# Kernel optimization log

Hardware: AMD Instinct MI355X
Metric: run time of the kernel (lower is better)

The kernel has to match this reference:

```python
import jax, jax.numpy as jnp
import numpy as np

D_MODEL = 1024
NUM_HEADS = 16
HEAD_DIM = D_MODEL // NUM_HEADS
B, S = 4, 2048


def _xavier(key, shape, gain=0.1):
    fan_in, fan_out = shape[1], shape[0]
    a = gain * np.sqrt(6.0 / (fan_in + fan_out))
    return jax.random.uniform(key, shape, jnp.float32, -a, a)


def setup_inputs() -> dict:
    key = jax.random.key(0)
    ks = jax.random.split(key, 11)
    inp = {
        "q": jax.random.normal(ks[0], (B, S, D_MODEL), jnp.float32),
        "k": jax.random.normal(ks[1], (B, S, D_MODEL), jnp.float32),
        "v": jax.random.normal(ks[2], (B, S, D_MODEL), jnp.float32),
        # nn.Linear weights are [out, in]; y = x @ W.T + b
        "Wq": _xavier(ks[3], (D_MODEL, D_MODEL)),
        "bq": jnp.zeros((D_MODEL,), jnp.float32),
        "Wk": _xavier(ks[4], (D_MODEL, D_MODEL)),
        "bk": jnp.zeros((D_MODEL,), jnp.float32),
        "Wv": _xavier(ks[5], (D_MODEL, D_MODEL)),
        "bv": jnp.zeros((D_MODEL,), jnp.float32),
        "Wo": _xavier(ks[6], (D_MODEL, D_MODEL)),
        "bo": jnp.zeros((D_MODEL,), jnp.float32),
    }
    return inp


def reference(q, k, v, Wq, bq, Wk, bk, Wv, bv, Wo, bo):
    b = q.shape[0]
    qh = (q @ Wq.T + bq).reshape(b, -1, NUM_HEADS, HEAD_DIM).transpose(0, 2, 1, 3)
    kh = (k @ Wk.T + bk).reshape(b, -1, NUM_HEADS, HEAD_DIM).transpose(0, 2, 1, 3)
    vh = (v @ Wv.T + bv).reshape(b, -1, NUM_HEADS, HEAD_DIM).transpose(0, 2, 1, 3)
    # NOTE: original (buggy) module scales by sqrt(d_model), not sqrt(head_dim)
    scale = 1.0 / jnp.sqrt(jnp.float32(D_MODEL))
    scores = jnp.einsum('bhqd,bhkd->bhqk', qh, kh) * scale  # [B,H,S,S]
    attn = jax.nn.softmax(scores, axis=-1)
    out = jnp.einsum('bhqk,bhkd->bhqd', attn, vh)
    out = out.transpose(0, 2, 1, 3).reshape(b, -1, D_MODEL)
    return out @ Wo.T + bo
```

## Files before the change

kernel.cpp:

```cpp
#include <hip/hip_runtime.h>

typedef unsigned short u16;
typedef short bf16x8 __attribute__((ext_vector_type(8)));
typedef float f32x4 __attribute__((ext_vector_type(4)));
typedef u16 u16x8 __attribute__((ext_vector_type(8)));

__device__ __forceinline__ u16 f2bf(float f) {
  unsigned u = __float_as_uint(f);
  u = u + 0x7fffu + ((u >> 16) & 1u);
  return (u16)(u >> 16);
}

__device__ __forceinline__ float fexp2(float x) {
#if __has_builtin(__builtin_amdgcn_exp2f)
  return __builtin_amdgcn_exp2f(x);
#else
  return exp2f(x);
#endif
}

#define GLD16(ldsp, gp)                                                         \
  __builtin_amdgcn_global_load_lds(                                             \
      (__attribute__((address_space(1))) void*)(void*)(gp),                     \
      (__attribute__((address_space(3))) void*)(ldsp), 16, 0, 0)

#define CVTPK(dst, lo, hi)                                                      \
  asm("v_cvt_pk_bf16_f32 %0, %1, %2" : "=v"(dst) : "v"(lo), "v"(hi))
#define PACK8(dst, a0, a1, a2, a3, a4, a5, a6, a7)                              \
  do {                                                                          \
    union { unsigned u_[4]; bf16x8 v_; } c_;                                    \
    CVTPK(c_.u_[0], a0, a1); CVTPK(c_.u_[1], a2, a3);                           \
    CVTPK(c_.u_[2], a4, a5); CVTPK(c_.u_[3], a6, a7);                           \
    dst = c_.v_;                                                                \
  } while (0)

__global__ __launch_bounds__(256) void pack_w4(const float* __restrict__ w0,
                                               const float* __restrict__ w1,
                                               const float* __restrict__ w2,
                                               const float* __restrict__ w3,
                                               u16* __restrict__ out) {
  int i = blockIdx.x * 256 + threadIdx.x;
  int which = i >> 17;
  const float* src = which == 0 ? w0 : which == 1 ? w1 : which == 2 ? w2 : w3;
  int j = i & 131071;
  const float4* p = (const float4*)src + (size_t)j * 2;
  float4 a = p[0], b = p[1];
  u16x8 r;
  r[0] = f2bf(a.x); r[1] = f2bf(a.y); r[2] = f2bf(a.z); r[3] = f2bf(a.w);
  r[4] = f2bf(b.x); r[5] = f2bf(b.y); r[6] = f2bf(b.z); r[7] = f2bf(b.w);
  *(u16x8*)(out + (size_t)i * 8) = r;
}

__global__ __launch_bounds__(256, 2)
void gemm_qkv(const float* __restrict__ qi, const float* __restrict__ ki,
              const float* __restrict__ vi, const u16* __restrict__ wbf,
              const float* __restrict__ bq, const float* __restrict__ bk,
              const float* __restrict__ bv, u16* __restrict__ qo,
              u16* __restrict__ ko, u16* __restrict__ vo) {
  constexpr int K = 1024;
  __shared__ __align__(16) u16 As[128 * 64];
  __shared__ __align__(16) u16 Bs[128 * 64];
  const int z = blockIdx.z;
  const float* Af = z == 0 ? qi : z == 1 ? ki : vi;
  const u16* Bw = wbf + ((size_t)z << 20);
  const float* bias = z == 0 ? bq : z == 1 ? bk : bv;

  const int t = threadIdx.x;
  const int w = t >> 6, l = t & 63;
  const int lr = l & 15, lg = l >> 4;
  const int flat = blockIdx.x | (blockIdx.y << 3);
  const int swz = ((flat & 7) << 6) | (flat >> 3);
  const int row0 = (swz >> 3) * 128, col0 = (swz & 7) * 128;
  const int wm = (w >> 1) * 64, wn = (w & 1) * 64;

  f32x4 acc[4][4] = {};

  const int ar = t >> 3;
  const int xw = ((t & 7) ^ (ar & 7)) * 16;
  const float* gA = Af + (size_t)(row0 + ar) * K + (t & 7) * 8;
  const u16* gB = Bw + (size_t)(col0 + ar) * K + (((t & 7) ^ (ar & 7)) * 8);
  u16* lB = &Bs[w * 512];

  float4 a0[4], a1[4];
#pragma unroll
  for (int j = 0; j < 4; ++j) {
    const float* p = gA + (size_t)j * 32 * K;
    a0[j] = *(const float4*)p;
    a1[j] = *(const float4*)(p + 4);
  }

  for (int kt = 0; kt < 16; ++kt) {
#pragma unroll
    for (int j = 0; j < 4; ++j) {
      bf16x8 c;
      PACK8(c, a0[j].x, a0[j].y, a0[j].z, a0[j].w, a1[j].x, a1[j].y, a1[j].z, a1[j].w);
      *(bf16x8*)((char*)As + (ar + j * 32) * 128 + xw) = c;
    }
#pragma unroll
    for (int j = 0; j < 4; ++j)
      GLD16(lB + j * 2048, gB + (size_t)j * 32 * K + kt * 64);
    if (kt < 15) {
#pragma unroll
      for (int j = 0; j < 4; ++j) {
        const float* p = gA + (size_t)j * 32 * K + (kt + 1) * 64;
        a0[j] = *(const float4*)p;
        a1[j] = *(const float4*)(p + 4);
      }
    }
    __syncthreads();
#pragma unroll
    for (int kh2 = 0; kh2 < 2; ++kh2) {
      bf16x8 aF[4], bF[4];
      const int bc = (kh2 * 64 + lg * 16) ^ ((lr & 7) * 16);
#pragma unroll
      for (int mi = 0; mi < 4; ++mi)
        aF[mi] = *(const bf16x8*)((const char*)As + (wm + mi * 16 + lr) * 128 + bc);
#pragma unroll
      for (int ni = 0; ni < 4; ++ni)
        bF[ni] = *(const bf16x8*)((const char*)Bs + (wn + ni * 16 + lr) * 128 + bc);
#pragma unroll
      for (int mi = 0; mi < 4; ++mi)
#pragma unroll
        for (int ni = 0; ni < 4; ++ni)
          acc[mi][ni] = __builtin_amdgcn_mfma_f32_16x16x32_bf16(aF[mi], bF[ni],
                                                                acc[mi][ni], 0, 0, 0);
    }
    __syncthreads();
  }

#pragma unroll
  for (int mi = 0; mi < 4; ++mi) {
#pragma unroll
    for (int ni = 0; ni < 4; ++ni) {
      const int n = col0 + wn + ni * 16 + lr;
      const float bvv = bias[n];
#pragma unroll
      for (int r = 0; r < 4; ++r) {
        const int m = row0 + wm + mi * 16 + lg * 4 + r;
        const float vv = acc[mi][ni][r] + bvv;
        const int bI = m >> 11, s = m & 2047, h = n >> 6, d = n & 63;
        if (z == 0) {
          qo[((size_t)((bI << 4) + h) * 2048 + s) * 64 + d] = f2bf(vv * 0.045084223f);
        } else if (z == 1) {
          ko[((size_t)((bI << 4) + h) * 2048 + s) * 64 + d] = f2bf(vv);
        } else {
          int bh = (bI << 4) + h, tile = s >> 6, kp = s & 63;
          int kM = kp >> 5, k5 = kp & 31;
          int kpp = kM * 32 + ((k5 >> 2) & 3) * 8 + (k5 >> 4) * 4 + (k5 & 3);
          int chunk = (kpp >> 3) ^ (d & 7);
          vo[((size_t)bh << 17) + tile * 4096 + d * 64 + chunk * 8 + (kpp & 7)] = f2bf(vv);
        }
      }
    }
  }
}

__global__ __launch_bounds__(256, 2)
void gemm_out(const u16* __restrict__ A, const u16* __restrict__ B,
              const float* __restrict__ bias, float* __restrict__ outp) {
  constexpr int K = 1024;
  __shared__ __align__(16) u16 As[128 * 64];
  __shared__ __align__(16) u16 Bs[128 * 64];
  const int t = threadIdx.x;
  const int w = t >> 6;
  const int l = t & 63;
  const int lr = l & 15, lg = l >> 4;
  const int flat = blockIdx.x | (blockIdx.y << 3);
  const int swz = ((flat & 7) << 6) | (flat >> 3);
  const int row0 = (swz >> 3) * 128, col0 = (swz & 7) * 128;
  const int wm = (w >> 1) * 64, wn = (w & 1) * 64;

  f32x4 acc[4][4] = {};

  const int srow = t >> 3;
  const int scol = ((t & 7) ^ (srow & 7)) * 8;
  const u16* gA = A + (size_t)(row0 + srow) * K + scol;
  const u16* gB = B + (size_t)(col0 + srow) * K + scol;
  u16* lA = &As[w * 512];
  u16* lB = &Bs[w * 512];

  for (int k0 = 0; k0 < K; k0 += 64) {
#pragma unroll
    for (int j = 0; j < 4; ++j) {
      GLD16(lA + j * 2048, gA + (size_t)j * 32 * K + k0);
      GLD16(lB + j * 2048, gB + (size_t)j * 32 * K + k0);
    }
    __syncthreads();
#pragma unroll
    for (int kh2 = 0; kh2 < 2; ++kh2) {
      bf16x8 aF[4], bF[4];
      const int bc = (kh2 * 64 + lg * 16) ^ ((lr & 7) * 16);
#pragma unroll
      for (int mi = 0; mi < 4; ++mi)
        aF[mi] = *(const bf16x8*)((const char*)As + (wm + mi * 16 + lr) * 128 + bc);
#pragma unroll
      for (int ni = 0; ni < 4; ++ni)
        bF[ni] = *(const bf16x8*)((const char*)Bs + (wn + ni * 16 + lr) * 128 + bc);
#pragma unroll
      for (int mi = 0; mi < 4; ++mi)
#pragma unroll
        for (int ni = 0; ni < 4; ++ni)
          acc[mi][ni] = __builtin_amdgcn_mfma_f32_16x16x32_bf16(aF[mi], bF[ni],
                                                                acc[mi][ni], 0, 0, 0);
    }
    __syncthreads();
  }

#pragma unroll
  for (int mi = 0; mi < 4; ++mi)
#pragma unroll
    for (int ni = 0; ni < 4; ++ni) {
      const int n = col0 + wn + ni * 16 + lr;
      const float bv = bias[n];
#pragma unroll
      for (int r = 0; r < 4; ++r) {
        const int m = row0 + wm + mi * 16 + lg * 4 + r;
        outp[(size_t)m * 1024 + n] = acc[mi][ni][r] + bv;
      }
    }
}

__global__ __launch_bounds__(256, 3)
void attn_fwd(const u16* __restrict__ qh, const u16* __restrict__ kh,
              const u16* __restrict__ vp, u16* __restrict__ aout) {
  __shared__ __align__(16) u16 Ks[2][4096];
  __shared__ __align__(16) u16 Vl[2][4096];
  const int t = threadIdx.x;
  const int w = t >> 6, l = t & 63;
  const int lr = l & 15, lg = l >> 4;
  const int flat = blockIdx.x | (blockIdx.y << 4);
  const int swz = ((flat & 7) << 7) | (flat >> 3);
  const int qb = swz & 15, bh = swz >> 4;
  const int q0 = qb * 128 + w * 32;

  bf16x8 qf[2][2];
#pragma unroll
  for (int qi = 0; qi < 2; ++qi) {
    const u16* qp = qh + ((size_t)bh * 2048 + q0 + qi * 16 + lr) * 64 + lg * 8;
    qf[qi][0] = *(const bf16x8*)qp;
    qf[qi][1] = *(const bf16x8*)(qp + 32);
  }

  f32x4 o0[4] = {}, o1[4] = {};
  f32x4 sm0 = {}, sm1 = {};
  const bf16x8 ones = {16256, 16256, 16256, 16256, 16256, 16256, 16256, 16256};

  const int krow = t >> 3, kseg = t & 7;
  const u16* gK = kh + ((size_t)bh * 2048 + krow) * 64 + ((kseg ^ (krow & 7)) * 8);
  const u16* gV = vp + ((size_t)bh << 17) + t * 8;

  const int xo0 = (lg * 16) ^ ((lr & 7) * 16);
  const int xo1 = xo0 ^ 64;

  {
    u16* kd = &Ks[0][0] + w * 512;
    u16* vd = &Vl[0][0] + w * 512;
    GLD16(kd, gK); GLD16(kd + 2048, gK + 2048);
    GLD16(vd, gV); GLD16(vd + 2048, gV + 2048);
    gK += 4096; gV += 4096;
  }
  __syncthreads();

  for (int tix = 0; tix < 32; ++tix) {
    const int cur = tix & 1;
    if (tix < 31) {
      u16* kd = &Ks[cur ^ 1][0] + w * 512;
      u16* vd = &Vl[cur ^ 1][0] + w * 512;
      GLD16(kd, gK); GLD16(kd + 2048, gK + 2048);
      GLD16(vd, gV); GLD16(vd + 2048, gV + 2048);
      gK += 4096; gV += 4096;
    }
    const char* kb = (const char*)&Ks[cur][0];
    f32x4 s0[4], s1[4];
    __builtin_amdgcn_s_setprio(1);
#pragma unroll
    for (int cq = 0; cq < 4; ++cq) {
      const char* rowp = kb + (cq * 16 + lr) * 128;
      bf16x8 kf0 = *(const bf16x8*)(rowp + xo0);
      bf16x8 kf1 = *(const bf16x8*)(rowp + xo1);
      f32x4 a = {}, b2 = {};
      a  = __builtin_amdgcn_mfma_f32_16x16x32_bf16(kf0, qf[0][0], a, 0, 0, 0);
      a  = __builtin_amdgcn_mfma_f32_16x16x32_bf16(kf1, qf[0][1], a, 0, 0, 0);
      b2 = __builtin_amdgcn_mfma_f32_16x16x32_bf16(kf0, qf[1][0], b2, 0, 0, 0);
      b2 = __builtin_amdgcn_mfma_f32_16x16x32_bf16(kf1, qf[1][1], b2, 0, 0, 0);
      s0[cq] = a; s1[cq] = b2;
    }
    __builtin_amdgcn_s_setprio(0);
    float p0[16], p1[16];
#pragma unroll
    for (int cq = 0; cq < 4; ++cq)
#pragma unroll
      for (int r = 0; r < 4; ++r) {
        p0[cq * 4 + r] = fexp2(s0[cq][r]);
        p1[cq * 4 + r] = fexp2(s1[cq][r]);
      }
    bf16x8 pA0, pA1, pB0, pB1;
    PACK8(pA0, p0[0], p0[1], p0[2], p0[3], p0[4], p0[5], p0[6], p0[7]);
    PACK8(pA1, p0[8], p0[9], p0[10], p0[11], p0[12], p0[13], p0[14], p0[15]);
    PACK8(pB0, p1[0], p1[1], p1[2], p1[3], p1[4], p1[5], p1[6], p1[7]);
    PACK8(pB1, p1[8], p1[9], p1[10], p1[11], p1[12], p1[13], p1[14], p1[15]);
    __builtin_amdgcn_s_setprio(1);
    sm0 = __builtin_amdgcn_mfma_f32_16x16x32_bf16(pA0, ones, sm0, 0, 0, 0);
    sm0 = __builtin_amdgcn_mfma_f32_16x16x32_bf16(pA1, ones, sm0, 0, 0, 0);
    sm1 = __builtin_amdgcn_mfma_f32_16x16x32_bf16(pB0, ones, sm1, 0, 0, 0);
    sm1 = __builtin_amdgcn_mfma_f32_16x16x32_bf16(pB1, ones, sm1, 0, 0, 0);
    const char* vbb = (const char*)&Vl[cur][0];
#pragma unroll
    for (int dc = 0; dc < 4; ++dc) {
      const char* rp = vbb + (dc * 16 + lr) * 128;
      bf16x8 vA = *(const bf16x8*)(rp + xo0);
      bf16x8 vB = *(const bf16x8*)(rp + xo1);
      o0[dc] = __builtin_amdgcn_mfma_f32_16x16x32_bf16(pA0, vA, o0[dc], 0, 0, 0);
      o0[dc] = __builtin_amdgcn_mfma_f32_16x16x32_bf16(pA1, vB, o0[dc], 0, 0, 0);
      o1[dc] = __builtin_amdgcn_mfma_f32_16x16x32_bf16(pB0, vA, o1[dc], 0, 0, 0);
      o1[dc] = __builtin_amdgcn_mfma_f32_16x16x32_bf16(pB1, vB, o1[dc], 0, 0, 0);
    }
    __builtin_amdgcn_s_setprio(0);
    __syncthreads();
  }

  const int b = bh >> 4, h = bh & 15;
#pragma unroll
  for (int r = 0; r < 4; ++r) {
    const float dA = 1.f / sm0[r];
    const float dB = 1.f / sm1[r];
    const size_t rowA = (size_t)b * 2048 + q0 + lg * 4 + r;
#pragma unroll
    for (int dc = 0; dc < 4; ++dc) {
      aout[rowA * 1024 + h * 64 + dc * 16 + lr] = f2bf(o0[dc][r] * dA);
      aout[(rowA + 16) * 1024 + h * 64 + dc * 16 + lr] = f2bf(o1[dc][r] * dB);
    }
  }
}

extern "C" void kernel_launch(void* const* d_in, const int* in_sizes, int n_in,
                              void* d_out, int out_size, void* d_ws, size_t ws_size,
                              hipStream_t stream) {
  const float* q  = (const float*)d_in[0];
  const float* k  = (const float*)d_in[1];
  const float* v  = (const float*)d_in[2];
  const float* Wq = (const float*)d_in[3];
  const float* bq = (const float*)d_in[4];
  const float* Wk = (const float*)d_in[5];
  const float* bk = (const float*)d_in[6];
  const float* Wv = (const float*)d_in[7];
  const float* bv = (const float*)d_in[8];
  const float* Wo = (const float*)d_in[9];
  const float* bo = (const float*)d_in[10];

  char* ws = (char*)d_ws;
  u16* wbf  = (u16*)(ws);
  u16* aout = (u16*)(ws + (8ull << 20));
  u16* qhB  = (u16*)(ws + (24ull << 20));
  u16* khB  = (u16*)(ws + (40ull << 20));
  u16* vtB  = (u16*)(ws + (56ull << 20));

  pack_w4<<<2048, 256, 0, stream>>>(Wq, Wk, Wv, Wo, wbf);
  gemm_qkv<<<dim3(8, 64, 3), 256, 0, stream>>>(q, k, v, wbf, bq, bk, bv,
                                               qhB, khB, vtB);
  attn_fwd<<<dim3(16, 64), 256, 0, stream>>>(qhB, khB, vtB, aout);
  gemm_out<<<dim3(8, 64), 256, 0, stream>>>(aout, wbf + (3u << 20), bo,
                                            (float*)d_out);

  (void)in_sizes; (void)n_in; (void)out_size; (void)ws_size;
}
```

Before: 172.1 us.

## Pre-convert activations to bf16 and run QKV projections as separate GEMMs

Replaces the fused QKV GEMM, which loaded fp32 activations through registers and packed them to bf16 in-kernel, with a standalone fp32-to-bf16 pack kernel followed by a templated bf16 GEMM per projection. The new GEMM loads both operands directly into LDS with global_load_lds. The intent is a simpler, more latency-tolerant inner loop. The cost is extra global traffic (writing and rereading bf16 activations), six launches instead of one, and the loss of the single 3-way grid, since the three projections now run serially through one shared buffer.

```diff
diff --git a/kernel.cpp b/kernel.cpp
--- a/kernel.cpp
+++ b/kernel.cpp
@@ -33,6 +33,18 @@
     CVTPK(c_.u_[2], a4, a5); CVTPK(c_.u_[3], a6, a7);                           \
     dst = c_.v_;                                                                \
   } while (0)
+
+__global__ __launch_bounds__(256) void pack_bf16(const float* __restrict__ in,
+                                                 u16* __restrict__ out, int n8) {
+  int i = blockIdx.x * blockDim.x + threadIdx.x;
+  if (i >= n8) return;
+  const float4* p = (const float4*)in + (size_t)i * 2;
+  float4 a = p[0], b = p[1];
+  u16x8 r;
+  r[0] = f2bf(a.x); r[1] = f2bf(a.y); r[2] = f2bf(a.z); r[3] = f2bf(a.w);
+  r[4] = f2bf(b.x); r[5] = f2bf(b.y); r[6] = f2bf(b.z); r[7] = f2bf(b.w);
+  *(u16x8*)(out + (size_t)i * 8) = r;
+}
 
 __global__ __launch_bounds__(256) void pack_w4(const float* __restrict__ w0,
                                                const float* __restrict__ w1,
@@ -51,22 +63,17 @@
   *(u16x8*)(out + (size_t)i * 8) = r;
 }
 
+template <int EPI>
 __global__ __launch_bounds__(256, 2)
-void gemm_qkv(const float* __restrict__ qi, const float* __restrict__ ki,
-              const float* __restrict__ vi, const u16* __restrict__ wbf,
-              const float* __restrict__ bq, const float* __restrict__ bk,
-              const float* __restrict__ bv, u16* __restrict__ qo,
-              u16* __restrict__ ko, u16* __restrict__ vo) {
+void gemm_bt(const u16* __restrict__ A, const u16* __restrict__ B,
+             const float* __restrict__ bias, u16* __restrict__ outp,
+             float qscale) {
   constexpr int K = 1024;
   __shared__ __align__(16) u16 As[128 * 64];
   __shared__ __align__(16) u16 Bs[128 * 64];
-  const int z = blockIdx.z;
-  const float* Af = z == 0 ? qi : z == 1 ? ki : vi;
-  const u16* Bw = wbf + ((size_t)z << 20);
-  const float* bias = z == 0 ? bq : z == 1 ? bk : bv;
-
   const int t = threadIdx.x;
-  const int w = t >> 6, l = t & 63;
+  const int w = t >> 6;
+  const int l = t & 63;
   const int lr = l & 15, lg = l >> 4;
   const int flat = blockIdx.x | (blockIdx.y << 3);
   const int swz = ((flat & 7) << 6) | (flat >> 3);
@@ -75,37 +82,18 @@
 
   f32x4 acc[4][4] = {};
 
-  const int ar = t >> 3;
-  const int xw = ((t & 7) ^ (ar & 7)) * 16;
-  const float* gA = Af + (size_t)(row0 + ar) * K + (t & 7) * 8;
-  const u16* gB = Bw + (size_t)(col0 + ar) * K + (((t & 7) ^ (ar & 7)) * 8);
+  const int srow = t >> 3;
+  const int scol = ((t & 7) ^ (srow & 7)) * 8;
+  const u16* gA = A + (size_t)(row0 + srow) * K + scol;
+  const u16* gB = B + (size_t)(col0 + srow) * K + scol;
+  u16* lA = &As[w * 512];
   u16* lB = &Bs[w * 512];
 
-  float4 a0[4], a1[4];
-#pragma unroll
-  for (int j = 0; j < 4; ++j) {
-    const float* p = gA + (size_t)j * 32 * K;
-    a0[j] = *(const float4*)p;
-    a1[j] = *(const float4*)(p + 4);
-  }
-
-  for (int kt = 0; kt < 16; ++kt) {
+  for (int k0 = 0; k0 < K; k0 += 64) {
 #pragma unroll
     for (int j = 0; j < 4; ++j) {
-      bf16x8 c;
-      PACK8(c, a0[j].x, a0[j].y, a0[j].z, a0[j].w, a1[j].x, a1[j].y, a1[j].z, a1[j].w);
-      *(bf16x8*)((char*)As + (ar + j * 32) * 128 + xw) = c;
-    }
-#pragma unroll
-    for (int j = 0; j < 4; ++j)
-      GLD16(lB + j * 2048, gB + (size_t)j * 32 * K + kt * 64);
-    if (kt < 15) {
-#pragma unroll
-      for (int j = 0; j < 4; ++j) {
-        const float* p = gA + (size_t)j * 32 * K + (kt + 1) * 64;
-        a0[j] = *(const float4*)p;
-        a1[j] = *(const float4*)(p + 4);
-      }
+      GLD16(lA + j * 2048, gA + (size_t)j * 32 * K + k0);
+      GLD16(lB + j * 2048, gB + (size_t)j * 32 * K + k0);
     }
     __syncthreads();
 #pragma unroll
@@ -133,22 +121,22 @@
 #pragma unroll
     for (int ni = 0; ni < 4; ++ni) {
       const int n = col0 + wn + ni * 16 + lr;
-      const float bvv = bias[n];
+      const float bv = bias[n];
 #pragma unroll
       for (int r = 0; r < 4; ++r) {
         const int m = row0 + wm + mi * 16 + lg * 4 + r;
-        const float vv = acc[mi][ni][r] + bvv;
-        const int bI = m >> 11, s = m & 2047, h = n >> 6, d = n & 63;
-        if (z == 0) {
-          qo[((size_t)((bI << 4) + h) * 2048 + s) * 64 + d] = f2bf(vv * 0.045084223f);
-        } else if (z == 1) {
-          ko[((size_t)((bI << 4) + h) * 2048 + s) * 64 + d] = f2bf(vv);
+        const float v = acc[mi][ni][r] + bv;
+        if (EPI == 0) {
+          int b = m >> 11, s = m & 2047, h = n >> 6, d = n & 63;
+          outp[((size_t)((b << 4) + h) * 2048 + s) * 64 + d] = f2bf(v * qscale);
         } else {
-          int bh = (bI << 4) + h, tile = s >> 6, kp = s & 63;
+          int b = m >> 11, s = m & 2047, h = n >> 6, d = n & 63;
+          int bh = (b << 4) + h, tile = s >> 6, kp = s & 63;
           int kM = kp >> 5, k5 = kp & 31;
           int kpp = kM * 32 + ((k5 >> 2) & 3) * 8 + (k5 >> 4) * 4 + (k5 & 3);
           int chunk = (kpp >> 3) ^ (d & 7);
-          vo[((size_t)bh << 17) + tile * 4096 + d * 64 + chunk * 8 + (kpp & 7)] = f2bf(vv);
+          outp[((size_t)bh << 17) + tile * 4096 + d * 64 + chunk * 8 + (kpp & 7)]
+              = f2bf(v);
         }
       }
     }
@@ -349,18 +337,25 @@
   const float* bo = (const float*)d_in[10];
 
   char* ws = (char*)d_ws;
-  u16* wbf  = (u16*)(ws);
-  u16* aout = (u16*)(ws + (8ull << 20));
-  u16* qhB  = (u16*)(ws + (24ull << 20));
-  u16* khB  = (u16*)(ws + (40ull << 20));
-  u16* vtB  = (u16*)(ws + (56ull << 20));
+  u16* wbf = (u16*)(ws);
+  u16* xbf = (u16*)(ws + (8ull << 20));
+  u16* qhB = (u16*)(ws + (24ull << 20));
+  u16* khB = (u16*)(ws + (40ull << 20));
+  u16* vtB = (u16*)(ws + (56ull << 20));
+  u16* aout = xbf;
 
   pack_w4<<<2048, 256, 0, stream>>>(Wq, Wk, Wv, Wo, wbf);
-  gemm_qkv<<<dim3(8, 64, 3), 256, 0, stream>>>(q, k, v, wbf, bq, bk, bv,
-                                               qhB, khB, vtB);
+
+  const int XN8 = 8192 * 1024 / 8;
+  dim3 gg(8, 64), gb(256);
+  pack_bf16<<<4096, 256, 0, stream>>>(q, xbf, XN8);
+  gemm_bt<0><<<gg, gb, 0, stream>>>(xbf, wbf + (0u << 20), bq, qhB, 0.045084223f);
+  pack_bf16<<<4096, 256, 0, stream>>>(k, xbf, XN8);
+  gemm_bt<0><<<gg, gb, 0, stream>>>(xbf, wbf + (1u << 20), bk, khB, 1.0f);
+  pack_bf16<<<4096, 256, 0, stream>>>(v, xbf, XN8);
+  gemm_bt<1><<<gg, gb, 0, stream>>>(xbf, wbf + (2u << 20), bv, vtB, 1.0f);
   attn_fwd<<<dim3(16, 64), 256, 0, stream>>>(qhB, khB, vtB, aout);
-  gemm_out<<<dim3(8, 64), 256, 0, stream>>>(aout, wbf + (3u << 20), bo,
-                                            (float*)d_out);
+  gemm_out<<<gg, gb, 0, stream>>>(aout, wbf + (3u << 20), bo, (float*)d_out);
 
   (void)in_sizes; (void)n_in; (void)out_size; (void)ws_size;
 }
```

Result: slower. 183.9 us (+6.9%).
